# Kernel tuning notes

Measured on AMD Instinct MI355X. Metric: run time of the kernel, lower is better.

The kernel has to match this reference:

```python
import jax, jax.numpy as jnp
import numpy as np

N_NODES = 100_000
N_EDGES = 3_200_000
N_FEAT = 128
N_HID = 8
N_CLASSES = 10


def setup_inputs() -> dict:
    key = jax.random.key(0)
    ks = jax.random.split(key, 16)
    g = lambda k, shape, fan_in: jax.random.normal(k, shape, jnp.float32) / np.sqrt(fan_in)
    inp = {}
    inp['x'] = jax.random.normal(ks[0], (N_NODES, N_FEAT), jnp.float32)
    inp['edge_index'] = jax.random.randint(ks[1], (2, N_EDGES), 0, N_NODES, jnp.int32)
    # lin: Linear(F, 8)
    inp['lin_w'] = g(ks[2], (N_FEAT, N_HID), N_FEAT)
    inp['lin_b'] = jnp.zeros((N_HID,), jnp.float32)
    # conv1: GATConv(8, 8, heads=2)
    inp['w1'] = g(ks[3], (N_HID, 2 * N_HID), N_HID)
    inp['a1_src'] = g(ks[4], (2, N_HID), N_HID)
    inp['a1_dst'] = g(ks[5], (2, N_HID), N_HID)
    inp['b1'] = jnp.zeros((2 * N_HID,), jnp.float32)
    # conv2: GATConv(16, 8, heads=2)
    inp['w2'] = g(ks[6], (2 * N_HID, 2 * N_HID), 2 * N_HID)
    inp['a2_src'] = g(ks[7], (2, N_HID), N_HID)
    inp['a2_dst'] = g(ks[8], (2, N_HID), N_HID)
    inp['b2'] = jnp.zeros((2 * N_HID,), jnp.float32)
    # conv3: GATConv(16, num_classes, heads=1, concat=False)
    inp['w3'] = g(ks[9], (2 * N_HID, N_CLASSES), 2 * N_HID)
    inp['a3_src'] = g(ks[10], (1, N_CLASSES), N_CLASSES)
    inp['a3_dst'] = g(ks[11], (1, N_CLASSES), N_CLASSES)
    inp['b3'] = jnp.zeros((N_CLASSES,), jnp.float32)
    return inp


def _gat_conv(x, W, a_src, a_dst, b, src, dst, heads, out_c, concat):
    """PyG GATConv with pre-appended self-loops in (src, dst)."""
    N = x.shape[0]
    xl = (x @ W).reshape(N, heads, out_c)                 # [N,H,C]
    alpha_src = (xl * a_src[None]).sum(-1)                # [N,H]
    alpha_dst = (xl * a_dst[None]).sum(-1)                # [N,H]
    e = jax.nn.leaky_relu(alpha_src[src] + alpha_dst[dst], 0.2)  # [E,H]
    # segment softmax over destination nodes
    m = jax.ops.segment_max(e, dst, num_segments=N)
    e = jnp.exp(e - m[dst])
    s = jax.ops.segment_sum(e, dst, num_segments=N)
    alpha = e / s[dst]                                    # [E,H]
    msg = xl[src] * alpha[:, :, None]                     # [E,H,C]
    out = jax.ops.segment_sum(msg, dst, num_segments=N)   # [N,H,C]
    out = out.reshape(N, heads * out_c) if concat else out.mean(axis=1)
    return out + b


def reference(x, edge_index, lin_w, lin_b, w1, a1_src, a1_dst, b1,
              w2, a2_src, a2_dst, b2, w3, a3_src, a3_dst, b3):
    N = x.shape[0]
    loops = jnp.arange(N, dtype=edge_index.dtype)
    src = jnp.concatenate([edge_index[0], loops])
    dst = jnp.concatenate([edge_index[1], loops])
    lrelu = lambda v: jax.nn.leaky_relu(v, 0.01)
    h = lrelu(x @ lin_w + lin_b)
    h = lrelu(_gat_conv(h, w1, a1_src, a1_dst, b1, src, dst, 2, N_HID, True))
    h = lrelu(_gat_conv(h, w2, a2_src, a2_dst, b2, src, dst, 2, N_HID, True))
    h = _gat_conv(h, w3, a3_src, a3_dst, b3, src, dst, 1, N_CLASSES, False)
    return jax.nn.log_softmax(h, axis=-1)
```

## Files before the change

### kernel.cpp

```cpp
#include <hip/hip_runtime.h>
#include <hip/hip_fp16.h>
#include <math.h>

#define N_NODES 100000
#define N_EDGES 3200000
#define ET (N_EDGES + N_NODES)
#define SLOT 80
#define KMAX 5
#define SHIFT 8
#define BNODES 256
#define NBUCK 391
#define BCAP 9088
#define P1_T 1024
#define E_PER 16
#define P1_WG ((N_EDGES + P1_T * E_PER - 1) / (P1_T * E_PER))
#define SCAN_T 1024
#define SCAN_CHUNK 98

__device__ __forceinline__ float lrelu(float v, float s) { return v > 0.f ? v : v * s; }

template <int CTRL>
__device__ __forceinline__ float dppmov(float v) {
    return __int_as_float(__builtin_amdgcn_update_dpp(0, __float_as_int(v), CTRL, 0xF, 0xF, true));
}

__device__ __forceinline__ void reduce16(float& v, float& ssum, float pa0, float pa1,
                                         float pa2, float pa3, int lane) {
    int b0 = lane & 1, b1 = (lane >> 1) & 1;
    float k0 = b0 ? pa2 : pa0, g0 = b0 ? pa0 : pa2;
    float k1 = b0 ? pa3 : pa1, g1 = b0 ? pa1 : pa3;
    float q0 = k0 + dppmov<0xB1>(g0);
    float q1 = k1 + dppmov<0xB1>(g1);
    float kk = b1 ? q1 : q0, gg = b1 ? q0 : q1;
    v = kk + dppmov<0x4E>(gg);
    v += __shfl_xor(v, 4, 64);
    v += __shfl_xor(v, 8, 64);
    ssum += dppmov<0xB1>(ssum);
    ssum += dppmov<0x4E>(ssum);
    ssum += __shfl_xor(ssum, 4, 64);
    ssum += __shfl_xor(ssum, 8, 64);
}

__global__ __launch_bounds__(256) void lin_kernel(const float* __restrict__ x,
                                                  const float* __restrict__ w,
                                                  const float* __restrict__ b,
                                                  float* __restrict__ h0) {
    int lane = threadIdx.x & 63;
    int wid = blockIdx.x * 4 + (threadIdx.x >> 6);
    float4 wa0 = *(const float4*)&w[lane * 8];
    float4 wa1 = *(const float4*)&w[lane * 8 + 4];
    float4 wb0 = *(const float4*)&w[(lane + 64) * 8];
    float4 wb1 = *(const float4*)&w[(lane + 64) * 8 + 4];
    float wk0[8] = {wa0.x, wa0.y, wa0.z, wa0.w, wa1.x, wa1.y, wa1.z, wa1.w};
    float wk1[8] = {wb0.x, wb0.y, wb0.z, wb0.w, wb1.x, wb1.y, wb1.z, wb1.w};
    int l = lane & 7;
    int kmap = 4 * (l & 1) + 2 * ((l >> 1) & 1) + ((l >> 2) & 1);
    float bk = b[kmap];
#pragma unroll
    for (int j = 0; j < 4; j++) {
        int n = wid * 4 + j;
        if (n >= N_NODES) break;
        float x0 = x[n * 128 + lane];
        float x1 = x[n * 128 + 64 + lane];
        float acc[8];
#pragma unroll
        for (int k = 0; k < 8; k++) acc[k] = x0 * wk0[k] + x1 * wk1[k];
#pragma unroll
        for (int k = 0; k < 4; k++) {
            float keep = (lane & 1) ? acc[k + 4] : acc[k];
            float give = (lane & 1) ? acc[k] : acc[k + 4];
            acc[k] = keep + __shfl_xor(give, 1, 64);
        }
#pragma unroll
        for (int k = 0; k < 2; k++) {
            float keep = (lane & 2) ? acc[k + 2] : acc[k];
            float give = (lane & 2) ? acc[k] : acc[k + 2];
            acc[k] = keep + __shfl_xor(give, 2, 64);
        }
        {
            float keep = (lane & 4) ? acc[1] : acc[0];
            float give = (lane & 4) ? acc[0] : acc[1];
            acc[0] = keep + __shfl_xor(give, 4, 64);
        }
        acc[0] += __shfl_xor(acc[0], 8, 64);
        acc[0] += __shfl_xor(acc[0], 16, 64);
        acc[0] += __shfl_xor(acc[0], 32, 64);
        if (lane < 8) h0[n * 8 + kmap] = lrelu(acc[0] + bk, 0.01f);
    }
}

__global__ void __launch_bounds__(P1_T) part_kernel(const int* __restrict__ ei,
                                                    int* __restrict__ bcur,
                                                    unsigned* __restrict__ pairs) {
    __shared__ int hist[NBUCK];
    __shared__ int gbase[NBUCK];
    int t = threadIdx.x;
    for (int i = t; i < NBUCK; i += P1_T) hist[i] = 0;
    __syncthreads();
    int base = blockIdx.x * (P1_T * E_PER);
    int s[E_PER], d[E_PER], r[E_PER];
#pragma unroll
    for (int k = 0; k < E_PER; k++) {
        int e = base + k * P1_T + t;
        if (e < N_EDGES) {
            s[k] = ei[e];
            d[k] = ei[N_EDGES + e];
            r[k] = atomicAdd(&hist[d[k] >> SHIFT], 1);
        }
    }
    __syncthreads();
    for (int i = t; i < NBUCK; i += P1_T)
        gbase[i] = (hist[i] > 0) ? atomicAdd(&bcur[i], hist[i]) : 0;
    __syncthreads();
#pragma unroll
    for (int k = 0; k < E_PER; k++) {
        int e = base + k * P1_T + t;
        if (e < N_EDGES) {
            int b = d[k] >> SHIFT;
            int pos = gbase[b] + r[k];
            if (pos < BCAP)
                pairs[(size_t)b * BCAP + pos] =
                    ((unsigned)(d[k] & (BNODES - 1)) << 17) | (unsigned)s[k];
        }
    }
}

__global__ void build_kernel(const int* __restrict__ bcur, const unsigned* __restrict__ pairs,
                             int* __restrict__ csr, int* __restrict__ deg) {
    __shared__ int offs[BNODES];
    int b = blockIdx.x;
    int t = threadIdx.x;
    int node0 = b << SHIFT;
    int n = node0 + t;
    if (n < N_NODES) {
        csr[n * SLOT] = n;
        offs[t] = 1;
    } else offs[t] = 0;
    __syncthreads();
    int cnt = min(bcur[b], BCAP);
    for (int i = t; i < cnt; i += BNODES) {
        unsigned v = pairs[(size_t)b * BCAP + i];
        int ln = v >> 17;
        int s = v & 0x1FFFF;
        int pos = atomicAdd(&offs[ln], 1);
        if (pos < SLOT) csr[(node0 + ln) * SLOT + pos] = s;
    }
    __syncthreads();
    if (n < N_NODES) deg[n] = offs[t];
}

__global__ void count_kernel(const int* __restrict__ ei, int* __restrict__ deg) {
    int e = blockIdx.x * blockDim.x + threadIdx.x;
    if (e >= ET) return;
    int d = (e < N_EDGES) ? ei[N_EDGES + e] : (e - N_EDGES);
    atomicAdd(&deg[d], 1);
}

__global__ void scan_kernel(const int* __restrict__ deg, int* __restrict__ rowptr,
                            int* __restrict__ cursor) {
    __shared__ int sums[SCAN_T];
    int t = threadIdx.x;
    int start = t * SCAN_CHUNK;
    int end = min(start + SCAN_CHUNK, N_NODES);
    int s = 0;
    for (int i = start; i < end; i++) s += deg[i];
    sums[t] = s;
    __syncthreads();
    for (int off = 1; off < SCAN_T; off <<= 1) {
        int v = sums[t];
        int add = (t >= off) ? sums[t - off] : 0;
        __syncthreads();
        sums[t] = v + add;
        __syncthreads();
    }
    int base = (t > 0) ? sums[t - 1] : 0;
    for (int i = start; i < end; i++) {
        rowptr[i] = base;
        cursor[i] = base;
        base += deg[i];
    }
    if (t == SCAN_T - 1) rowptr[N_NODES] = base;
}

__global__ void scatter_kernel(const int* __restrict__ ei, int* __restrict__ cursor,
                               int* __restrict__ csr) {
    int e = blockIdx.x * blockDim.x + threadIdx.x;
    if (e >= ET) return;
    int s, d;
    if (e < N_EDGES) { s = ei[e]; d = ei[N_EDGES + e]; } else { s = d = e - N_EDGES; }
    int pos = atomicAdd(&cursor[d], 1);
    csr[pos] = s;
}

template <int CIN, int H, int C, int XLS>
__global__ void prep_kernel(const float* __restrict__ hin, const float* __restrict__ W,
                            const float* __restrict__ a_src, const float* __restrict__ a_dst,
                            __half* __restrict__ xl, float* __restrict__ asrc,
                            float* __restrict__ adst) {
    __shared__ float Ws[CIN * H * C];
    __shared__ float As[H * C];
    __shared__ float Ad[H * C];
    for (int i = threadIdx.x; i < CIN * H * C; i += blockDim.x) Ws[i] = W[i];
    for (int i = threadIdx.x; i < H * C; i += blockDim.x) { As[i] = a_src[i]; Ad[i] = a_dst[i]; }
    __syncthreads();
    int n = blockIdx.x * blockDim.x + threadIdx.x;
    if (n >= N_NODES) return;
    float hreg[CIN];
#pragma unroll
    for (int i = 0; i < CIN; i += 4) {
        float4 v = *(const float4*)&hin[n * CIN + i];
        hreg[i] = v.x; hreg[i + 1] = v.y; hreg[i + 2] = v.z; hreg[i + 3] = v.w;
    }
#pragma unroll
    for (int h = 0; h < H; h++) {
        float as = 0.f, ad = 0.f;
#pragma unroll
        for (int c = 0; c < C; c++) {
            float v = 0.f;
#pragma unroll
            for (int i = 0; i < CIN; i++) v += hreg[i] * Ws[i * H * C + h * C + c];
            xl[n * XLS + h * C + c] = __float2half_rn(v);
            as += v * As[h * C + c];
            ad += v * Ad[h * C + c];
        }
        asrc[n * H + h] = as;
        adst[n * H + h] = ad;
    }
#pragma unroll
    for (int c = H * C; c < XLS; c++) xl[n * XLS + c] = __float2half_rn(0.f);
}

__global__ __launch_bounds__(256) void gat64_h2(const int* __restrict__ cnt_,
                                                const int* __restrict__ csr,
                                                const float* __restrict__ asrc,
                                                const float* __restrict__ adst,
                                                const __half* __restrict__ xl,
                                                const float* __restrict__ b,
                                                float* __restrict__ hout) {
    int wg = blockIdx.x * 4 + (threadIdx.x >> 6);
    int lane = threadIdx.x & 63;
    int eg = lane & 15;
    int cp = lane >> 4;
    int h = cp >> 1;
    int n0 = wg * 2, n1 = n0 + 1;
    int cnt0 = min(cnt_[n0], SLOT);
    int cnt1 = min(cnt_[n1], SLOT);
    float ad0 = adst[n0 * 2 + h];
    float ad1 = adst[n1 * 2 + h];
    int idx0[KMAX], idx1[KMAX];
#pragma unroll
    for (int k = 0; k < KMAX; k++) {
        int i = eg + (k << 4);
        idx0[k] = (i < cnt0) ? csr[n0 * SLOT + i] : -1;
        idx1[k] = (i < cnt1) ? csr[n1 * SLOT + i] : -1;
    }
    float s0 = 0.f, a00 = 0.f, a01 = 0.f, a02 = 0.f, a03 = 0.f;
    float s1 = 0.f, a10 = 0.f, a11 = 0.f, a12 = 0.f, a13 = 0.f;
#pragma unroll
    for (int k = 0; k < KMAX; k++) {
        int s = idx0[k];
        if (s >= 0) {
            float e = asrc[s * 2 + h] + ad0;
            float w = __expf(fmaxf(e, 0.2f * e));
            float2 raw = *(const float2*)&xl[s * 16 + 4 * cp];
            float2 f01 = __half22float2(*(__half2*)&raw.x);
            float2 f23 = __half22float2(*(__half2*)&raw.y);
            s0 += w;
            a00 += w * f01.x; a01 += w * f01.y; a02 += w * f23.x; a03 += w * f23.y;
        }
        int t = idx1[k];
        if (t >= 0) {
            float e = asrc[t * 2 + h] + ad1;
            float w = __expf(fmaxf(e, 0.2f * e));
            float2 raw = *(const float2*)&xl[t * 16 + 4 * cp];
            float2 f01 = __half22float2(*(__half2*)&raw.x);
            float2 f23 = __half22float2(*(__half2*)&raw.y);
            s1 += w;
            a10 += w * f01.x; a11 += w * f01.y; a12 += w * f23.x; a13 += w * f23.y;
        }
    }
    float v0, v1;
    reduce16(v0, s0, a00, a01, a02, a03, lane);
    reduce16(v1, s1, a10, a11, a12, a13, lane);
    if ((lane & 12) == 0) {
        int ch = 4 * cp + 2 * (lane & 1) + ((lane >> 1) & 1);
        float bc = b[ch];
        hout[n0 * 16 + ch] = lrelu(v0 / s0 + bc, 0.01f);
        hout[n1 * 16 + ch] = lrelu(v1 / s1 + bc, 0.01f);
    }
}

__global__ __launch_bounds__(256) void gat64_ls(const int* __restrict__ cnt_,
                                                const int* __restrict__ csr,
                                                const float* __restrict__ asrc,
                                                const float* __restrict__ adst,
                                                const __half* __restrict__ xl,
                                                const float* __restrict__ b,
                                                float* __restrict__ out) {
    int wg = blockIdx.x * 4 + (threadIdx.x >> 6);
    int lane = threadIdx.x & 63;
    int eg = lane & 15;
    int cp = lane >> 4;
    int n0 = wg * 2, n1 = n0 + 1;
    int cnt0 = min(cnt_[n0], SLOT);
    int cnt1 = min(cnt_[n1], SLOT);
    float ad0 = adst[n0];
    float ad1 = adst[n1];
    int idx0[KMAX], idx1[KMAX];
#pragma unroll
    for (int k = 0; k < KMAX; k++) {
        int i = eg + (k << 4);
        idx0[k] = (i < cnt0) ? csr[n0 * SLOT + i] : -1;
        idx1[k] = (i < cnt1) ? csr[n1 * SLOT + i] : -1;
    }
    float s0 = 0.f, a00 = 0.f, a01 = 0.f, a02 = 0.f, a03 = 0.f;
    float s1 = 0.f, a10 = 0.f, a11 = 0.f, a12 = 0.f, a13 = 0.f;
#pragma unroll
    for (int k = 0; k < KMAX; k++) {
        int s = idx0[k];
        if (s >= 0) {
            float e = asrc[s] + ad0;
            float w = __expf(fmaxf(e, 0.2f * e));
            float2 raw = *(const float2*)&xl[s * 16 + 4 * cp];
            float2 f01 = __half22float2(*(__half2*)&raw.x);
            float2 f23 = __half22float2(*(__half2*)&raw.y);
            s0 += w;
            a00 += w * f01.x; a01 += w * f01.y; a02 += w * f23.x; a03 += w * f23.y;
        }
        int t = idx1[k];
        if (t >= 0) {
            float e = asrc[t] + ad1;
            float w = __expf(fmaxf(e, 0.2f * e));
            float2 raw = *(const float2*)&xl[t * 16 + 4 * cp];
            float2 f01 = __half22float2(*(__half2*)&raw.x);
            float2 f23 = __half22float2(*(__half2*)&raw.y);
            s1 += w;
            a10 += w * f01.x; a11 += w * f01.y; a12 += w * f23.x; a13 += w * f23.y;
        }
    }
    float v0, v1;
    reduce16(v0, s0, a00, a01, a02, a03, lane);
    reduce16(v1, s1, a10, a11, a12, a13, lane);
    int ch = 4 * cp + 2 * (lane & 1) + ((lane >> 1) & 1);
    float bc = (ch < 10) ? b[ch] : 0.f;
    float u0 = (ch < 10) ? v0 / s0 + bc : -INFINITY;
    float u1 = (ch < 10) ? v1 / s1 + bc : -INFINITY;
    float m0 = u0, m1 = u1;
    m0 = fmaxf(m0, dppmov<0xB1>(m0)); m1 = fmaxf(m1, dppmov<0xB1>(m1));
    m0 = fmaxf(m0, dppmov<0x4E>(m0)); m1 = fmaxf(m1, dppmov<0x4E>(m1));
    m0 = fmaxf(m0, __shfl_xor(m0, 16, 64)); m1 = fmaxf(m1, __shfl_xor(m1, 16, 64));
    m0 = fmaxf(m0, __shfl_xor(m0, 32, 64)); m1 = fmaxf(m1, __shfl_xor(m1, 32, 64));
    float e0 = (ch < 10) ? __expf(u0 - m0) : 0.f;
    float e1 = (ch < 10) ? __expf(u1 - m1) : 0.f;
    e0 += dppmov<0xB1>(e0); e1 += dppmov<0xB1>(e1);
    e0 += dppmov<0x4E>(e0); e1 += dppmov<0x4E>(e1);
    e0 += __shfl_xor(e0, 16, 64); e1 += __shfl_xor(e1, 16, 64);
    e0 += __shfl_xor(e0, 32, 64); e1 += __shfl_xor(e1, 32, 64);
    float lse0 = m0 + __logf(e0);
    float lse1 = m1 + __logf(e1);
    if ((lane & 12) == 0 && ch < 10) {
        out[n0 * 10 + ch] = u0 - lse0;
        out[n1 * 10 + ch] = u1 - lse1;
    }
}

__global__ void gat16_h2(const int* __restrict__ rowptr, const int* __restrict__ csr,
                         const float* __restrict__ asrc, const float* __restrict__ adst,
                         const __half* __restrict__ xl, const float* __restrict__ b,
                         float* __restrict__ hout) {
    int tid = blockIdx.x * blockDim.x + threadIdx.x;
    int wave = tid >> 6;
    int lane = threadIdx.x & 63;
    int g = lane >> 4;
    int c = lane & 15;
    int h = c >> 3;
    int n = wave * 4 + g;
    if (n >= N_NODES) return;
    int beg = rowptr[n], cnt = rowptr[n + 1] - beg;
    float adn = adst[n * 2 + h];
    float ssum = 0.f, pa = 0.f;
#pragma unroll 4
    for (int i = 0; i < cnt; i++) {
        int s = csr[beg + i];
        float e = asrc[s * 2 + h] + adn;
        float w = __expf(fmaxf(e, 0.2f * e));
        ssum += w;
        pa += w * __half2float(xl[s * 16 + c]);
    }
    hout[n * 16 + c] = lrelu(pa / ssum + b[c], 0.01f);
}

__global__ void gat16_ls(const int* __restrict__ rowptr, const int* __restrict__ csr,
                         const float* __restrict__ asrc, const float* __restrict__ adst,
                         const __half* __restrict__ xl, const float* __restrict__ b,
                         float* __restrict__ out) {
    int tid = blockIdx.x * blockDim.x + threadIdx.x;
    int wave = tid >> 6;
    int lane = threadIdx.x & 63;
    int g = lane >> 4;
    int c = lane & 15;
    int n = wave * 4 + g;
    if (n >= N_NODES) return;
    int beg = rowptr[n], cnt = rowptr[n + 1] - beg;
    float adn = adst[n];
    float ssum = 0.f, pa = 0.f;
#pragma unroll 4
    for (int i = 0; i < cnt; i++) {
        int s = csr[beg + i];
        float e = asrc[s] + adn;
        float w = __expf(fmaxf(e, 0.2f * e));
        ssum += w;
        pa += w * __half2float(xl[s * 16 + c]);
    }
    float v = pa / ssum + ((c < 10) ? b[c] : 0.f);
    float vm = (c < 10) ? v : -INFINITY;
#pragma unroll
    for (int off = 8; off >= 1; off >>= 1) vm = fmaxf(vm, __shfl_xor(vm, off, 16));
    float ex = (c < 10) ? __expf(v - vm) : 0.f;
    float sum = ex;
#pragma unroll
    for (int off = 8; off >= 1; off >>= 1) sum += __shfl_xor(sum, off, 16);
    float lse = vm + __logf(sum);
    if (c < 10) out[n * 10 + c] = v - lse;
}

extern "C" void kernel_launch(void* const* d_in, const int* in_sizes, int n_in,
                              void* d_out, int out_size, void* d_ws, size_t ws_size,
                              hipStream_t stream) {
    const float* x     = (const float*)d_in[0];
    const int*   ei    = (const int*)d_in[1];
    const float* lin_w = (const float*)d_in[2];
    const float* lin_b = (const float*)d_in[3];
    const float* w1    = (const float*)d_in[4];
    const float* a1s   = (const float*)d_in[5];
    const float* a1d   = (const float*)d_in[6];
    const float* b1    = (const float*)d_in[7];
    const float* w2    = (const float*)d_in[8];
    const float* a2s   = (const float*)d_in[9];
    const float* a2d   = (const float*)d_in[10];
    const float* b2    = (const float*)d_in[11];
    const float* w3    = (const float*)d_in[12];
    const float* a3s   = (const float*)d_in[13];
    const float* a3d   = (const float*)d_in[14];
    const float* b3    = (const float*)d_in[15];

    float* ws = (float*)d_ws;
    float* slotH  = ws;
    __half* slotX = (__half*)(ws + 1600000);
    float* as_    = ws + 3200000;
    float* ad_    = ws + 3400000;
    unsigned* pairs = (unsigned*)ws;
    int* csrP = (int*)(ws + 3600000);
    int* degP = (int*)(ws + 3600000 + N_NODES * SLOT);
    int* bcur = degP + N_NODES;
    size_t need_new = (size_t)(3600000 + N_NODES * SLOT + N_NODES + 512) * 4;

    int use_bucket = (ws_size >= need_new) ? 1 : 0;

    int* degC    = (int*)(ws + 3600000);
    int* rowptrC = degC + N_NODES;
    int* cursorC = rowptrC + N_NODES + 1;
    int* csrC    = cursorC + N_NODES;

    dim3 B(256);
    int nb_n  = (N_NODES + 255) / 256;
    int nb_et = (ET + 255) / 256;
    int nb_g  = (N_NODES + 15) / 16;
    int nb_w2 = N_NODES / 8;

    if (use_bucket) {
        hipMemsetAsync(bcur, 0, 512 * sizeof(int), stream);
        part_kernel<<<P1_WG, P1_T, 0, stream>>>(ei, bcur, pairs);
        build_kernel<<<NBUCK, BNODES, 0, stream>>>(bcur, pairs, csrP, degP);
    } else {
        hipMemsetAsync(degC, 0, N_NODES * sizeof(int), stream);
        count_kernel<<<nb_et, B, 0, stream>>>(ei, degC);
        scan_kernel<<<1, SCAN_T, 0, stream>>>(degC, rowptrC, cursorC);
        scatter_kernel<<<nb_et, B, 0, stream>>>(ei, cursorC, csrC);
    }

    lin_kernel<<<dim3((N_NODES + 15) / 16), B, 0, stream>>>(x, lin_w, lin_b, slotH);

    prep_kernel<8, 2, 8, 16><<<nb_n, B, 0, stream>>>(slotH, w1, a1s, a1d, slotX, as_, ad_);
    if (use_bucket) gat64_h2<<<nb_w2, B, 0, stream>>>(degP, csrP, as_, ad_, slotX, b1, slotH);
    else            gat16_h2<<<nb_g, B, 0, stream>>>(rowptrC, csrC, as_, ad_, slotX, b1, slotH);

    prep_kernel<16, 2, 8, 16><<<nb_n, B, 0, stream>>>(slotH, w2, a2s, a2d, slotX, as_, ad_);
    if (use_bucket) gat64_h2<<<nb_w2, B, 0, stream>>>(degP, csrP, as_, ad_, slotX, b2, slotH);
    else            gat16_h2<<<nb_g, B, 0, stream>>>(rowptrC, csrC, as_, ad_, slotX, b2, slotH);

    prep_kernel<16, 1, 10, 16><<<nb_n, B, 0, stream>>>(slotH, w3, a3s, a3d, slotX, as_, ad_);
    if (use_bucket) gat64_ls<<<nb_w2, B, 0, stream>>>(degP, csrP, as_, ad_, slotX, b3, (float*)d_out);
    else            gat16_ls<<<nb_g, B, 0, stream>>>(rowptrC, csrC, as_, ad_, slotX, b3, (float*)d_out);
}
```

Measured before the change: 331.4 us.

## Recompute source attention logits from gathered features; split prep across two threads per node

The GAT aggregation kernels for layers 1 and 2 no longer gather the per-source attention scalar. Each lane takes a dot product of its gathered half-precision features with a_src and combines with its neighbour lane through a shuffle, trading one random global load per edge for a few FMAs and a cross-lane shuffle. The prep kernels now use two threads per node (one per head or half of the columns) and write xl as a single vectorized 16-byte store, which raises parallelism and coalescing. The recomputed logit uses fp16-rounded features, so it can differ slightly from the fp32 value computed before.

```diff
diff --git a/kernel.cpp b/kernel.cpp
--- a/kernel.cpp
+++ b/kernel.cpp
@@ -192,18 +192,23 @@
     csr[pos] = s;
 }
 
-template <int CIN, int H, int C, int XLS>
-__global__ void prep_kernel(const float* __restrict__ hin, const float* __restrict__ W,
-                            const float* __restrict__ a_src, const float* __restrict__ a_dst,
-                            __half* __restrict__ xl, float* __restrict__ asrc,
-                            float* __restrict__ adst) {
-    __shared__ float Ws[CIN * H * C];
-    __shared__ float As[H * C];
-    __shared__ float Ad[H * C];
-    for (int i = threadIdx.x; i < CIN * H * C; i += blockDim.x) Ws[i] = W[i];
-    for (int i = threadIdx.x; i < H * C; i += blockDim.x) { As[i] = a_src[i]; Ad[i] = a_dst[i]; }
-    __syncthreads();
-    int n = blockIdx.x * blockDim.x + threadIdx.x;
+template <int CIN>
+__global__ __launch_bounds__(256) void prep_h2(const float* __restrict__ hin,
+                                               const float* __restrict__ W,
+                                               const float* __restrict__ a_src,
+                                               const float* __restrict__ a_dst,
+                                               __half* __restrict__ xl,
+                                               float* __restrict__ asrc,
+                                               float* __restrict__ adst) {
+    __shared__ float Ws[CIN * 16];
+    __shared__ float As[16];
+    __shared__ float Ad[16];
+    for (int i = threadIdx.x; i < CIN * 16; i += blockDim.x) Ws[i] = W[i];
+    if (threadIdx.x < 16) { As[threadIdx.x] = a_src[threadIdx.x]; Ad[threadIdx.x] = a_dst[threadIdx.x]; }
+    __syncthreads();
+    int t = blockIdx.x * blockDim.x + threadIdx.x;
+    int n = t >> 1;
+    int h = t & 1;
     if (n >= N_NODES) return;
     float hreg[CIN];
 #pragma unroll
@@ -211,28 +216,72 @@
         float4 v = *(const float4*)&hin[n * CIN + i];
         hreg[i] = v.x; hreg[i + 1] = v.y; hreg[i + 2] = v.z; hreg[i + 3] = v.w;
     }
-#pragma unroll
-    for (int h = 0; h < H; h++) {
-        float as = 0.f, ad = 0.f;
-#pragma unroll
-        for (int c = 0; c < C; c++) {
-            float v = 0.f;
-#pragma unroll
-            for (int i = 0; i < CIN; i++) v += hreg[i] * Ws[i * H * C + h * C + c];
-            xl[n * XLS + h * C + c] = __float2half_rn(v);
-            as += v * As[h * C + c];
-            ad += v * Ad[h * C + c];
-        }
-        asrc[n * H + h] = as;
-        adst[n * H + h] = ad;
-    }
-#pragma unroll
-    for (int c = H * C; c < XLS; c++) xl[n * XLS + c] = __float2half_rn(0.f);
+    float as = 0.f, ad = 0.f;
+    __half hv[8];
+#pragma unroll
+    for (int c = 0; c < 8; c++) {
+        int col = h * 8 + c;
+        float v = 0.f;
+#pragma unroll
+        for (int i = 0; i < CIN; i++) v += hreg[i] * Ws[i * 16 + col];
+        hv[c] = __float2half_rn(v);
+        as += v * As[col];
+        ad += v * Ad[col];
+    }
+    *(float4*)&xl[n * 16 + h * 8] = *(float4*)hv;
+    asrc[n * 2 + h] = as;
+    adst[n * 2 + h] = ad;
+}
+
+__global__ __launch_bounds__(256) void prep_c3(const float* __restrict__ hin,
+                                               const float* __restrict__ W,
+                                               const float* __restrict__ a_src,
+                                               const float* __restrict__ a_dst,
+                                               __half* __restrict__ xl,
+                                               float* __restrict__ asrc,
+                                               float* __restrict__ adst) {
+    __shared__ float Ws[16 * 10];
+    __shared__ float As[10];
+    __shared__ float Ad[10];
+    for (int i = threadIdx.x; i < 160; i += blockDim.x) Ws[i] = W[i];
+    if (threadIdx.x < 10) { As[threadIdx.x] = a_src[threadIdx.x]; Ad[threadIdx.x] = a_dst[threadIdx.x]; }
+    __syncthreads();
+    int t = blockIdx.x * blockDim.x + threadIdx.x;
+    int n = t >> 1;
+    int hf = t & 1;
+    if (n >= N_NODES) return;
+    float hreg[16];
+#pragma unroll
+    for (int i = 0; i < 16; i += 4) {
+        float4 v = *(const float4*)&hin[n * 16 + i];
+        hreg[i] = v.x; hreg[i + 1] = v.y; hreg[i + 2] = v.z; hreg[i + 3] = v.w;
+    }
+    float as = 0.f, ad = 0.f;
+    __half hv[8];
+#pragma unroll
+    for (int c = 0; c < 8; c++) {
+        int col = hf * 8 + c;
+        float v = 0.f;
+        if (col < 10) {
+#pragma unroll
+            for (int i = 0; i < 16; i++) v += hreg[i] * Ws[i * 10 + col];
+            as += v * As[col];
+            ad += v * Ad[col];
+        }
+        hv[c] = __float2half_rn(v);
+    }
+    *(float4*)&xl[n * 16 + hf * 8] = *(float4*)hv;
+    as += __shfl_xor(as, 1, 64);
+    ad += __shfl_xor(ad, 1, 64);
+    if (hf == 0) {
+        asrc[n] = as;
+        adst[n] = ad;
+    }
 }
 
 __global__ __launch_bounds__(256) void gat64_h2(const int* __restrict__ cnt_,
                                                 const int* __restrict__ csr,
-                                                const float* __restrict__ asrc,
+                                                const float* __restrict__ a_src,
                                                 const float* __restrict__ adst,
                                                 const __half* __restrict__ xl,
                                                 const float* __restrict__ b,
@@ -243,6 +292,7 @@
     int cp = lane >> 4;
     int h = cp >> 1;
     int n0 = wg * 2, n1 = n0 + 1;
+    float4 asv = *(const float4*)&a_src[4 * cp];
     int cnt0 = min(cnt_[n0], SLOT);
     int cnt1 = min(cnt_[n1], SLOT);
     float ad0 = adst[n0 * 2 + h];
@@ -260,21 +310,25 @@
     for (int k = 0; k < KMAX; k++) {
         int s = idx0[k];
         if (s >= 0) {
-            float e = asrc[s * 2 + h] + ad0;
-            float w = __expf(fmaxf(e, 0.2f * e));
             float2 raw = *(const float2*)&xl[s * 16 + 4 * cp];
             float2 f01 = __half22float2(*(__half2*)&raw.x);
             float2 f23 = __half22float2(*(__half2*)&raw.y);
+            float part = f01.x * asv.x + f01.y * asv.y + f23.x * asv.z + f23.y * asv.w;
+            float as = part + __shfl_xor(part, 16, 64);
+            float e = as + ad0;
+            float w = __expf(fmaxf(e, 0.2f * e));
             s0 += w;
             a00 += w * f01.x; a01 += w * f01.y; a02 += w * f23.x; a03 += w * f23.y;
         }
         int t = idx1[k];
         if (t >= 0) {
-            float e = asrc[t * 2 + h] + ad1;
-            float w = __expf(fmaxf(e, 0.2f * e));
             float2 raw = *(const float2*)&xl[t * 16 + 4 * cp];
             float2 f01 = __half22float2(*(__half2*)&raw.x);
             float2 f23 = __half22float2(*(__half2*)&raw.y);
+            float part = f01.x * asv.x + f01.y * asv.y + f23.x * asv.z + f23.y * asv.w;
+            float as = part + __shfl_xor(part, 16, 64);
+            float e = as + ad1;
+            float w = __expf(fmaxf(e, 0.2f * e));
             s1 += w;
             a10 += w * f01.x; a11 += w * f01.y; a12 += w * f23.x; a13 += w * f23.y;
         }
@@ -463,9 +517,9 @@
     int* csrC    = cursorC + N_NODES;
 
     dim3 B(256);
-    int nb_n  = (N_NODES + 255) / 256;
     int nb_et = (ET + 255) / 256;
     int nb_g  = (N_NODES + 15) / 16;
+    int nb_p  = (2 * N_NODES + 255) / 256;
     int nb_w2 = N_NODES / 8;
 
     if (use_bucket) {
@@ -481,15 +535,15 @@
 
     lin_kernel<<<dim3((N_NODES + 15) / 16), B, 0, stream>>>(x, lin_w, lin_b, slotH);
 
-    prep_kernel<8, 2, 8, 16><<<nb_n, B, 0, stream>>>(slotH, w1, a1s, a1d, slotX, as_, ad_);
-    if (use_bucket) gat64_h2<<<nb_w2, B, 0, stream>>>(degP, csrP, as_, ad_, slotX, b1, slotH);
+    prep_h2<8><<<nb_p, B, 0, stream>>>(slotH, w1, a1s, a1d, slotX, as_, ad_);
+    if (use_bucket) gat64_h2<<<nb_w2, B, 0, stream>>>(degP, csrP, a1s, ad_, slotX, b1, slotH);
     else            gat16_h2<<<nb_g, B, 0, stream>>>(rowptrC, csrC, as_, ad_, slotX, b1, slotH);
 
-    prep_kernel<16, 2, 8, 16><<<nb_n, B, 0, stream>>>(slotH, w2, a2s, a2d, slotX, as_, ad_);
-    if (use_bucket) gat64_h2<<<nb_w2, B, 0, stream>>>(degP, csrP, as_, ad_, slotX, b2, slotH);
+    prep_h2<16><<<nb_p, B, 0, stream>>>(slotH, w2, a2s, a2d, slotX, as_, ad_);
+    if (use_bucket) gat64_h2<<<nb_w2, B, 0, stream>>>(degP, csrP, a2s, ad_, slotX, b2, slotH);
     else            gat16_h2<<<nb_g, B, 0, stream>>>(rowptrC, csrC, as_, ad_, slotX, b2, slotH);
 
-    prep_kernel<16, 1, 10, 16><<<nb_n, B, 0, stream>>>(slotH, w3, a3s, a3d, slotX, as_, ad_);
+    prep_c3<<<nb_p, B, 0, stream>>>(slotH, w3, a3s, a3d, slotX, as_, ad_);
     if (use_bucket) gat64_ls<<<nb_w2, B, 0, stream>>>(degP, csrP, as_, ad_, slotX, b3, (float*)d_out);
     else            gat16_ls<<<nb_g, B, 0, stream>>>(rowptrC, csrC, as_, ad_, slotX, b3, (float*)d_out);
 }
```

New measurement: 307.1 us. 1.08x faster.
